# Performance work log

Hardware: AMD Instinct MI355X
Metric: run time of the kernel (lower is better)

The kernel has to match this reference:

```python
import jax, jax.numpy as jnp
import numpy as np

N_NODES = 100000
N_EDGES = 3200000
IN_DIM = 256
HID_DIM = 64
OUT_DIM = 64


def setup_inputs() -> dict:
    key = jax.random.key(0)
    k1, k2, k3, k4, k5, k6 = jax.random.split(key, 6)
    x = jax.random.normal(k1, (N_NODES, IN_DIM), dtype=jnp.float32)
    edge_index = jax.random.randint(k2, (2, N_EDGES), 0, N_NODES, dtype=jnp.int32)
    # Glorot-style init for the two GCNConv layers (PyG default: glorot weight, zero bias)
    W1 = jax.random.normal(k3, (IN_DIM, HID_DIM), dtype=jnp.float32) * (1.0 / np.sqrt(IN_DIM))
    b1 = jnp.zeros((HID_DIM,), dtype=jnp.float32)
    W2 = jax.random.normal(k4, (HID_DIM, OUT_DIM), dtype=jnp.float32) * (1.0 / np.sqrt(HID_DIM))
    b2 = jnp.zeros((OUT_DIM,), dtype=jnp.float32)
    return {"x": x, "edge_index": edge_index, "W1": W1, "b1": b1, "W2": W2, "b2": b2}


def _gcn_conv(x, src, dst, deg_inv_sqrt, W, b, n):
    # PyG GCNConv: h = x W; out_i = sum_j norm_ij * h_j + b, with symmetric norm
    h = x @ W                                   # (n, d_out) small GEMM
    norm = deg_inv_sqrt[src] * deg_inv_sqrt[dst]  # (E+n,)
    msg = norm[:, None] * h[src]                # gather (E+n, d_out)
    agg = jax.ops.segment_sum(msg, dst, num_segments=n)  # scatter-add
    return agg + b


def reference(x, edge_index, W1, b1, W2, b2):
    n = x.shape[0]
    loops = jnp.arange(n, dtype=edge_index.dtype)
    src = jnp.concatenate([edge_index[0], loops])
    dst = jnp.concatenate([edge_index[1], loops])
    # degree on destination (col) with added self-loops, weight 1.0
    deg = jax.ops.segment_sum(jnp.ones_like(dst, dtype=x.dtype), dst, num_segments=n)
    deg_inv_sqrt = jnp.where(deg > 0, jax.lax.rsqrt(deg), 0.0)
    h = jax.nn.relu(_gcn_conv(x, src, dst, deg_inv_sqrt, W1, b1, n))
    return _gcn_conv(h, src, dst, deg_inv_sqrt, W2, b2, n)
```

## Files before the change

kernel.cpp:

```cpp
#include <hip/hip_runtime.h>
#include <cstdint>
#include <cstddef>


#define BIN_SHIFT 7
#define BIN_NODES 128
#define MAX_BINS 1024
#define SUP_SHIFT 11
#define FINE_PER_SUP 16
#define NSUP_MAX 64
#define SCAP 56
#define SRC_BITS 17
#define SRC_MASK ((1 << SRC_BITS) - 1)

typedef unsigned short ushort_t;

typedef __attribute__((ext_vector_type(8))) short bf16x8;
typedef __attribute__((ext_vector_type(4))) float f32x4;

union FragB {
  uint4 u;
  bf16x8 b;
};

__device__ __forceinline__ float4 bfq2f4(uint2 p) {
  float4 r;
  r.x = __uint_as_float(p.x << 16);
  r.y = __uint_as_float(p.x & 0xFFFF0000u);
  r.z = __uint_as_float(p.y << 16);
  r.w = __uint_as_float(p.y & 0xFFFF0000u);
  return r;
}
__device__ __forceinline__ unsigned f2bf(float f) {
  unsigned u = __float_as_uint(f);
  return (u + 0x7FFFu + ((u >> 16) & 1u)) >> 16;
}
__device__ __forceinline__ uint2 f42bfq(float4 f) {
  uint2 r;
  r.x = f2bf(f.x) | (f2bf(f.y) << 16);
  r.y = f2bf(f.z) | (f2bf(f.w) << 16);
  return r;
}

__global__ void zero_int(int* __restrict__ p, int n) {
  int i = blockIdx.x * blockDim.x + threadIdx.x;
  if (i < n) p[i] = 0;
}

__global__ __launch_bounds__(256) void bin_count(const int* __restrict__ dst, int E, int nbins,
                                                 int* __restrict__ binCnt) {
  __shared__ int h[MAX_BINS];
  for (int i = threadIdx.x; i < nbins; i += 256) h[i] = 0;
  __syncthreads();
  int stride = gridDim.x * 256;
  for (int e = blockIdx.x * 256 + threadIdx.x; e < E; e += stride)
    atomicAdd(&h[dst[e] >> BIN_SHIFT], 1);
  __syncthreads();
  for (int i = threadIdx.x; i < nbins; i += 256)
    if (h[i]) atomicAdd(&binCnt[i], h[i]);
}

__global__ __launch_bounds__(256) void bin_scan(const int* __restrict__ binCnt, int nbins, int E,
                                                int* __restrict__ binStart,
                                                int* __restrict__ binCursor,
                                                int* __restrict__ supCursor) {
  __shared__ int s[256];
  int t = threadIdx.x;
  int c[4];
  int sum = 0;
#pragma unroll
  for (int i = 0; i < 4; i++) {
    int idx = t * 4 + i;
    c[i] = (idx < nbins) ? binCnt[idx] : 0;
    sum += c[i];
  }
  int v = sum;
  s[t] = v;
  __syncthreads();
  for (int d = 1; d < 256; d <<= 1) {
    int add = (t >= d) ? s[t - d] : 0;
    __syncthreads();
    s[t] += add;
    __syncthreads();
  }
  int run = s[t] - v;
#pragma unroll
  for (int i = 0; i < 4; i++) {
    int idx = t * 4 + i;
    if (idx < nbins) {
      binStart[idx] = run;
      binCursor[idx] = run;
      if ((idx & (FINE_PER_SUP - 1)) == 0) supCursor[idx >> 4] = run;
      run += c[i];
    }
  }
  if (t == 0) binStart[nbins] = E;
}

__global__ __launch_bounds__(256) void super_fill(const int* __restrict__ src,
                                                  const int* __restrict__ dst, int E, int nsup,
                                                  int* __restrict__ supCursor,
                                                  unsigned* __restrict__ supbuf) {
  __shared__ unsigned stage[NSUP_MAX * SCAP];
  __shared__ int lcnt[NSUP_MAX], lbase[NSUP_MAX], lscan[NSUP_MAX + 1];
  int chunk = (E + gridDim.x - 1) / gridDim.x;
  int c0 = blockIdx.x * chunk;
  int c1 = min(E, c0 + chunk);
  for (int t0 = c0; t0 < c1; t0 += 2048) {
    int t1 = min(c1, t0 + 2048);
    if (threadIdx.x < nsup) lcnt[threadIdx.x] = 0;
    __syncthreads();
    for (int e = t0 + threadIdx.x; e < t1; e += 256) {
      int d = dst[e];
      int sb = d >> SUP_SHIFT;
      unsigned v = ((unsigned)(d & ((1 << SUP_SHIFT) - 1)) << SRC_BITS) | (unsigned)src[e];
      int idx = atomicAdd(&lcnt[sb], 1);
      if (idx < SCAP)
        stage[sb * SCAP + idx] = v;
      else {
        int g = atomicAdd(&supCursor[sb], 1);
        supbuf[g] = v;
      }
    }
    __syncthreads();
    if (threadIdx.x < nsup) {
      int c = min(lcnt[threadIdx.x], SCAP);
      lcnt[threadIdx.x] = c;
      lbase[threadIdx.x] = c ? atomicAdd(&supCursor[threadIdx.x], c) : 0;
    }
    __syncthreads();
    if (threadIdx.x == 0) {
      int r = 0;
      for (int i = 0; i < nsup; i++) {
        lscan[i] = r;
        r += lcnt[i];
      }
      lscan[nsup] = r;
    }
    __syncthreads();
    int total = lscan[nsup];
    for (int j = threadIdx.x; j < total; j += 256) {
      int lo = 0, hi = nsup;
      while (hi - lo > 1) {
        int mid = (lo + hi) >> 1;
        if (lscan[mid] <= j)
          lo = mid;
        else
          hi = mid;
      }
      int off = j - lscan[lo];
      supbuf[lbase[lo] + off] = stage[lo * SCAP + off];
    }
    __syncthreads();
  }
}

__global__ __launch_bounds__(256) void fine_fill(const unsigned* __restrict__ supbuf,
                                                 const int* __restrict__ binStart, int nbins,
                                                 int* __restrict__ binCursor,
                                                 unsigned* __restrict__ binbuf) {
  __shared__ int lcnt[FINE_PER_SUP], lbase[FINE_PER_SUP];
  int sb = blockIdx.x >> 3, p = blockIdx.x & 7;
  int seg0 = binStart[sb << 4];
  int seg1 = binStart[min((sb + 1) << 4, nbins)];
  int part = (seg1 - seg0 + 7) >> 3;
  int c0 = seg0 + p * part;
  int c1 = min(seg1, c0 + part);
  if (threadIdx.x < FINE_PER_SUP) lcnt[threadIdx.x] = 0;
  __syncthreads();
  for (int i = c0 + threadIdx.x; i < c1; i += 256) atomicAdd(&lcnt[supbuf[i] >> 24], 1);
  __syncthreads();
  if (threadIdx.x < FINE_PER_SUP) {
    int c = lcnt[threadIdx.x];
    lbase[threadIdx.x] = c ? atomicAdd(&binCursor[(sb << 4) + threadIdx.x], c) : 0;
    lcnt[threadIdx.x] = 0;
  }
  __syncthreads();
  for (int i = c0 + threadIdx.x; i < c1; i += 256) {
    unsigned v = supbuf[i];
    unsigned dls = v >> SRC_BITS;
    int f = dls >> BIN_SHIFT;
    unsigned vf = ((dls & (BIN_NODES - 1)) << SRC_BITS) | (v & SRC_MASK);
    int idx = lbase[f] + atomicAdd(&lcnt[f], 1);
    binbuf[idx] = vf;
  }
}

__global__ __launch_bounds__(256) void node_count_dis(const unsigned* __restrict__ binbuf,
                                                      const int* __restrict__ binStart, int N,
                                                      int* __restrict__ count,
                                                      float* __restrict__ dis) {
  __shared__ int cnt[BIN_NODES];
  int b = blockIdx.x;
  int nodeBase = b << BIN_SHIFT;
  if (threadIdx.x < BIN_NODES) cnt[threadIdx.x] = 0;
  __syncthreads();
  int s0 = binStart[b], s1 = binStart[b + 1];
  for (int i = s0 + threadIdx.x; i < s1; i += 256) atomicAdd(&cnt[binbuf[i] >> SRC_BITS], 1);
  __syncthreads();
  if (threadIdx.x < BIN_NODES) {
    int node = nodeBase + threadIdx.x;
    if (node < N) {
      int c = cnt[threadIdx.x];
      count[node] = c;
      dis[node] = rsqrtf((float)(c + 1));
    }
  }
}

__global__ __launch_bounds__(256) void bin_csr(const unsigned* __restrict__ binbuf,
                                               const int* __restrict__ binStart,
                                               const int* __restrict__ count, int N, int E,
                                               int* __restrict__ rowptr, int* __restrict__ col) {
  __shared__ int cur[BIN_NODES];
  __shared__ int pref[BIN_NODES];
  int b = blockIdx.x, t = threadIdx.x;
  int nodeBase = b << BIN_SHIFT;
  int c = 0;
  if (t < BIN_NODES) {
    int node = nodeBase + t;
    c = (node < N) ? count[node] : 0;
    pref[t] = c;
  }
  __syncthreads();
  for (int d = 1; d < BIN_NODES; d <<= 1) {
    int add = (t < BIN_NODES && t >= d) ? pref[t - d] : 0;
    __syncthreads();
    if (t < BIN_NODES) pref[t] += add;
    __syncthreads();
  }
  int s0 = binStart[b];
  if (t < BIN_NODES) {
    int node = nodeBase + t;
    if (node < N) {
      int ex = s0 + pref[t] - c;
      rowptr[node] = ex;
      cur[t] = ex;
    }
  }
  if (b == 0 && t == 255) rowptr[N] = E;
  __syncthreads();
  int s1 = binStart[b + 1];
  for (int i = s0 + t; i < s1; i += 256) {
    unsigned v = binbuf[i];
    int slot = atomicAdd(&cur[v >> SRC_BITS], 1);
    col[slot] = v & SRC_MASK;
  }
}

__global__ __launch_bounds__(256) void wsplit(const float* __restrict__ W1,
                                              const float* __restrict__ W2,
                                              ushort_t* __restrict__ wt1,
                                              ushort_t* __restrict__ wt2) {
  int i = blockIdx.x * 256 + threadIdx.x;
  const float* W;
  ushort_t* wt;
  int K, idx;
  if (i < 256 * 64) {
    W = W1; wt = wt1; K = 256; idx = i;
  } else if (i < 256 * 64 + 64 * 64) {
    W = W2; wt = wt2; K = 64; idx = i - 256 * 64;
  } else
    return;
  int n = idx & 63, k = idx >> 6;
  float f = W[k * 64 + n];
  unsigned u = __float_as_uint(f);
  unsigned hb = u & 0xFFFF0000u;
  float lo = f - __uint_as_float(hb);
  wt[(size_t)n * K + k] = (ushort_t)(u >> 16);
  wt[(size_t)64 * K + (size_t)n * K + k] = (ushort_t)(__float_as_uint(lo) >> 16);
}

__device__ __forceinline__ void split8(const float* __restrict__ xp, uint4& xh, uint4& xl) {
  float f[8];
  *(float4*)&f[0] = *(const float4*)xp;
  *(float4*)&f[4] = *(const float4*)(xp + 4);
  unsigned hw[4], lw[4];
#pragma unroll
  for (int p = 0; p < 4; p++) {
    unsigned ua = __float_as_uint(f[2 * p]);
    unsigned ub = __float_as_uint(f[2 * p + 1]);
    unsigned ha = ua & 0xFFFF0000u;
    unsigned hb = ub & 0xFFFF0000u;
    float la = f[2 * p] - __uint_as_float(ha);
    float lb = f[2 * p + 1] - __uint_as_float(hb);
    hw[p] = (ua >> 16) | hb;
    lw[p] = (__float_as_uint(la) >> 16) | (__float_as_uint(lb) & 0xFFFF0000u);
  }
  xh = make_uint4(hw[0], hw[1], hw[2], hw[3]);
  xl = make_uint4(lw[0], lw[1], lw[2], lw[3]);
}

template <int K, bool ABF16>
__global__ __launch_bounds__(256) void gemm_mfma(const void* __restrict__ Av,
                                                 const ushort_t* __restrict__ Wt,
                                                 uint2* __restrict__ Cb, int M) {
  const int lane = threadIdx.x & 63;
  const int wv = threadIdx.x >> 6;
  const int l15 = lane & 15;
  const int lq = lane >> 4;
  const int m0 = blockIdx.x * 128 + wv * 32;

  const ushort_t* __restrict__ Wlo = Wt + (size_t)64 * K;

  f32x4 acc[2][4];
#pragma unroll
  for (int a = 0; a < 2; a++)
#pragma unroll
    for (int b = 0; b < 4; b++) acc[a][b] = (f32x4){0.f, 0.f, 0.f, 0.f};

  int node[2], ncl[2];
#pragma unroll
  for (int mt = 0; mt < 2; mt++) {
    node[mt] = m0 + mt * 16 + l15;
    ncl[mt] = node[mt] < M ? node[mt] : (M - 1);
  }

#pragma unroll 2
  for (int kt = 0; kt < K / 32; kt++) {
    const int kb = kt * 32 + lq * 8;
    FragB wh[4], wl[4];
#pragma unroll
    for (int nt = 0; nt < 4; nt++) {
      wh[nt].u = *(const uint4*)(Wt + (size_t)(nt * 16 + l15) * K + kb);
      wl[nt].u = *(const uint4*)(Wlo + (size_t)(nt * 16 + l15) * K + kb);
    }
#pragma unroll
    for (int mt = 0; mt < 2; mt++) {
      if (ABF16) {
        FragB xa;
        xa.u = *(const uint4*)((const ushort_t*)Av + (size_t)ncl[mt] * K + kb);
#pragma unroll
        for (int nt = 0; nt < 4; nt++) {
          acc[mt][nt] =
              __builtin_amdgcn_mfma_f32_16x16x32_bf16(wh[nt].b, xa.b, acc[mt][nt], 0, 0, 0);
          acc[mt][nt] =
              __builtin_amdgcn_mfma_f32_16x16x32_bf16(wl[nt].b, xa.b, acc[mt][nt], 0, 0, 0);
        }
      } else {
        FragB xh, xl;
        split8((const float*)Av + (size_t)ncl[mt] * K + kb, xh.u, xl.u);
#pragma unroll
        for (int nt = 0; nt < 4; nt++) {
          acc[mt][nt] =
              __builtin_amdgcn_mfma_f32_16x16x32_bf16(wh[nt].b, xh.b, acc[mt][nt], 0, 0, 0);
          acc[mt][nt] =
              __builtin_amdgcn_mfma_f32_16x16x32_bf16(wl[nt].b, xh.b, acc[mt][nt], 0, 0, 0);
          acc[mt][nt] =
              __builtin_amdgcn_mfma_f32_16x16x32_bf16(wh[nt].b, xl.b, acc[mt][nt], 0, 0, 0);
        }
      }
    }
  }

#pragma unroll
  for (int mt = 0; mt < 2; mt++) {
    if (node[mt] < M) {
      uint2* cp = Cb + (size_t)node[mt] * 16 + lq;
#pragma unroll
      for (int nt = 0; nt < 4; nt++) {
        float4 o = make_float4(acc[mt][nt][0], acc[mt][nt][1], acc[mt][nt][2], acc[mt][nt][3]);
        cp[nt * 4] = f42bfq(o);
      }
    }
  }
}

template <bool OUTBF>
__global__ __launch_bounds__(256) void agg_kernel(
    const uint2* __restrict__ h, const int* __restrict__ rowptr, const int* __restrict__ col,
    const float* __restrict__ dis, const float* __restrict__ bias, void* __restrict__ outv,
    int N, int relu) {
  int wid = (blockIdx.x * blockDim.x + threadIdx.x) >> 6;
  if (wid >= N) return;
  int lane = threadIdx.x & 63;
  int sub = lane & 15;
  int quarter = lane >> 4;

  int start = rowptr[wid], end = rowptr[wid + 1];
  float di = dis[wid];

  float4 a0 = make_float4(0.f, 0.f, 0.f, 0.f), a1 = a0, a2 = a0, a3 = a0;
  {
    float4 self = bfq2f4(h[(size_t)wid * 16 + sub]);
    if (quarter == 0) {
      a0.x = di * self.x;
      a0.y = di * self.y;
      a0.z = di * self.z;
      a0.w = di * self.w;
    }
  }

  for (int base = start; base < end; base += 64) {
    int e = base + lane;
    int sj = 0;
    float wj = 0.f;
    if (e < end) {
      sj = col[e];
      wj = dis[sj];
    }
    int cnt = end - base;
    if (cnt > 64) cnt = 64;
    int rounds = (cnt + 3) >> 2;
    int t = 0;
    for (; t + 4 <= rounds; t += 4) {
      int i0 = 4 * t + quarter;
      int s0 = __shfl(sj, i0), s1 = __shfl(sj, i0 + 4), s2 = __shfl(sj, i0 + 8),
          s3 = __shfl(sj, i0 + 12);
      float w0 = __shfl(wj, i0), w1 = __shfl(wj, i0 + 4), w2 = __shfl(wj, i0 + 8),
            w3 = __shfl(wj, i0 + 12);
      float4 g0 = bfq2f4(h[(size_t)s0 * 16 + sub]);
      float4 g1 = bfq2f4(h[(size_t)s1 * 16 + sub]);
      float4 g2 = bfq2f4(h[(size_t)s2 * 16 + sub]);
      float4 g3 = bfq2f4(h[(size_t)s3 * 16 + sub]);
      a0.x += w0 * g0.x; a0.y += w0 * g0.y; a0.z += w0 * g0.z; a0.w += w0 * g0.w;
      a1.x += w1 * g1.x; a1.y += w1 * g1.y; a1.z += w1 * g1.z; a1.w += w1 * g1.w;
      a2.x += w2 * g2.x; a2.y += w2 * g2.y; a2.z += w2 * g2.z; a2.w += w2 * g2.w;
      a3.x += w3 * g3.x; a3.y += w3 * g3.y; a3.z += w3 * g3.z; a3.w += w3 * g3.w;
    }
    for (; t < rounds; t++) {
      int i0 = 4 * t + quarter;
      int s0 = __shfl(sj, i0);
      float w0 = __shfl(wj, i0);
      float4 g0 = bfq2f4(h[(size_t)s0 * 16 + sub]);
      a0.x += w0 * g0.x; a0.y += w0 * g0.y; a0.z += w0 * g0.z; a0.w += w0 * g0.w;
    }
  }

  float sx = (a0.x + a1.x) + (a2.x + a3.x);
  float sy = (a0.y + a1.y) + (a2.y + a3.y);
  float sz = (a0.z + a1.z) + (a2.z + a3.z);
  float sw = (a0.w + a1.w) + (a2.w + a3.w);
  sx += __shfl_down(sx, 32); sy += __shfl_down(sy, 32);
  sz += __shfl_down(sz, 32); sw += __shfl_down(sw, 32);
  sx += __shfl_down(sx, 16); sy += __shfl_down(sy, 16);
  sz += __shfl_down(sz, 16); sw += __shfl_down(sw, 16);
  if (quarter == 0) {
    float4 bv = ((const float4*)bias)[sub];
    float4 o = make_float4(di * sx + bv.x, di * sy + bv.y, di * sz + bv.z, di * sw + bv.w);
    if (relu) {
      o.x = fmaxf(o.x, 0.f);
      o.y = fmaxf(o.y, 0.f);
      o.z = fmaxf(o.z, 0.f);
      o.w = fmaxf(o.w, 0.f);
    }
    if (OUTBF)
      ((uint2*)outv)[(size_t)wid * 16 + sub] = f42bfq(o);
    else
      ((float4*)outv)[(size_t)wid * 16 + sub] = o;
  }
}

extern "C" void kernel_launch(void* const* d_in, const int* in_sizes, int n_in,
                              void* d_out, int out_size, void* d_ws, size_t ws_size,
                              hipStream_t stream) {
  const float* x = (const float*)d_in[0];
  const int* ei = (const int*)d_in[1];
  const float* W1 = (const float*)d_in[2];
  const float* b1 = (const float*)d_in[3];
  const float* W2 = (const float*)d_in[4];
  const float* b2 = (const float*)d_in[5];

  const int IN = 256;
  const int E = in_sizes[1] / 2;
  const int N = in_sizes[0] / IN;
  const int* src = ei;
  const int* dst = ei + E;
  const int nbins = (N + BIN_NODES - 1) >> BIN_SHIFT;
  const int nsup = (N + (1 << SUP_SHIFT) - 1) >> SUP_SHIFT;

  char* ws = (char*)d_ws;
  size_t off = 0;
  auto alloc = [&](size_t bytes) -> void* {
    void* p = ws + off;
    off += (bytes + 255) & ~(size_t)255;
    return p;
  };
  int* count = (int*)alloc((size_t)N * 4);
  int* rowptr = (int*)alloc((size_t)(N + 1) * 4);
  float* dis = (float*)alloc((size_t)N * 4);
  int* binCnt = (int*)alloc(MAX_BINS * 4);
  int* binStart = (int*)alloc((MAX_BINS + 1) * 4);
  int* binCursor = (int*)alloc(MAX_BINS * 4);
  int* supCursor = (int*)alloc(NSUP_MAX * 4);
  int* col = (int*)alloc((size_t)E * 4);
  unsigned* supbuf = (unsigned*)col;
  uint2* out1 = (uint2*)alloc((size_t)N * 64 * 2);
  size_t big = ((size_t)E * 4 > (size_t)N * 128) ? (size_t)E * 4 : (size_t)N * 128;
  unsigned* binbuf = (unsigned*)alloc(big);
  uint2* h = (uint2*)binbuf;
  ushort_t* wt1 = (ushort_t*)alloc((size_t)2 * 64 * 256 * 2);
  ushort_t* wt2 = (ushort_t*)alloc((size_t)2 * 64 * 64 * 2);
  float* outf = (float*)d_out;

  zero_int<<<(nbins + 255) / 256, 256, 0, stream>>>(binCnt, nbins);
  bin_count<<<1024, 256, 0, stream>>>(dst, E, nbins, binCnt);
  bin_scan<<<1, 256, 0, stream>>>(binCnt, nbins, E, binStart, binCursor, supCursor);
  super_fill<<<512, 256, 0, stream>>>(src, dst, E, nsup, supCursor, supbuf);
  fine_fill<<<nsup * 8, 256, 0, stream>>>(supbuf, binStart, nbins, binCursor, binbuf);
  node_count_dis<<<nbins, 256, 0, stream>>>(binbuf, binStart, N, count, dis);
  bin_csr<<<nbins, 256, 0, stream>>>(binbuf, binStart, count, N, E, rowptr, col);
  wsplit<<<(256 * 64 + 64 * 64 + 255) / 256, 256, 0, stream>>>(W1, W2, wt1, wt2);

  gemm_mfma<256, false><<<(N + 127) / 128, 256, 0, stream>>>(x, wt1, h, N);
  agg_kernel<true><<<(N + 3) / 4, 256, 0, stream>>>(h, rowptr, col, dis, b1, out1, N, 1);
  gemm_mfma<64, true><<<(N + 127) / 128, 256, 0, stream>>>(out1, wt2, h, N);
  agg_kernel<false><<<(N + 3) / 4, 256, 0, stream>>>(h, rowptr, col, dis, b2, outf, N, 0);
}
```

Before: 476.6 us.

## Software-pipeline operand loads in MFMA GEMM and set occupancy bound

The fp32-input GEMM path now double-buffers the high weight fragments and prefetches the activation rows two K-steps ahead in registers, so global loads overlap the split and MFMA work. It also reorders the MFMAs to reuse each weight fragment across both M tiles. The bf16-input path hoists all K-step loads ahead of the MFMA chain. Launch bounds now request 3 blocks per CU, which caps registers against the larger register footprint and risks spills.

Result: no change. 473.9 us (-0.6%).

```diff
diff --git a/kernel.cpp b/kernel.cpp
--- a/kernel.cpp
+++ b/kernel.cpp
@@ -271,30 +271,26 @@
   wt[(size_t)64 * K + (size_t)n * K + k] = (ushort_t)(__float_as_uint(lo) >> 16);
 }
 
-__device__ __forceinline__ void split8(const float* __restrict__ xp, uint4& xh, uint4& xl) {
-  float f[8];
-  *(float4*)&f[0] = *(const float4*)xp;
-  *(float4*)&f[4] = *(const float4*)(xp + 4);
+__device__ __forceinline__ void split8u(uint4 a, uint4 b, uint4& xh, uint4& xl) {
+  unsigned ua[8] = {a.x, a.y, a.z, a.w, b.x, b.y, b.z, b.w};
   unsigned hw[4], lw[4];
 #pragma unroll
   for (int p = 0; p < 4; p++) {
-    unsigned ua = __float_as_uint(f[2 * p]);
-    unsigned ub = __float_as_uint(f[2 * p + 1]);
-    unsigned ha = ua & 0xFFFF0000u;
-    unsigned hb = ub & 0xFFFF0000u;
-    float la = f[2 * p] - __uint_as_float(ha);
-    float lb = f[2 * p + 1] - __uint_as_float(hb);
-    hw[p] = (ua >> 16) | hb;
-    lw[p] = (__float_as_uint(la) >> 16) | (__float_as_uint(lb) & 0xFFFF0000u);
+    unsigned u0 = ua[2 * p], u1 = ua[2 * p + 1];
+    unsigned h0 = u0 & 0xFFFF0000u, h1 = u1 & 0xFFFF0000u;
+    float l0 = __uint_as_float(u0) - __uint_as_float(h0);
+    float l1 = __uint_as_float(u1) - __uint_as_float(h1);
+    hw[p] = (u0 >> 16) | h1;
+    lw[p] = (__float_as_uint(l0) >> 16) | (__float_as_uint(l1) & 0xFFFF0000u);
   }
   xh = make_uint4(hw[0], hw[1], hw[2], hw[3]);
   xl = make_uint4(lw[0], lw[1], lw[2], lw[3]);
 }
 
 template <int K, bool ABF16>
-__global__ __launch_bounds__(256) void gemm_mfma(const void* __restrict__ Av,
-                                                 const ushort_t* __restrict__ Wt,
-                                                 uint2* __restrict__ Cb, int M) {
+__global__ __launch_bounds__(256, 3) void gemm_mfma(const void* __restrict__ Av,
+                                                    const ushort_t* __restrict__ Wt,
+                                                    uint2* __restrict__ Cb, int M) {
   const int lane = threadIdx.x & 63;
   const int wv = threadIdx.x >> 6;
   const int l15 = lane & 15;
@@ -316,39 +312,88 @@
     ncl[mt] = node[mt] < M ? node[mt] : (M - 1);
   }
 
-#pragma unroll 2
-  for (int kt = 0; kt < K / 32; kt++) {
-    const int kb = kt * 32 + lq * 8;
-    FragB wh[4], wl[4];
-#pragma unroll
-    for (int nt = 0; nt < 4; nt++) {
-      wh[nt].u = *(const uint4*)(Wt + (size_t)(nt * 16 + l15) * K + kb);
-      wl[nt].u = *(const uint4*)(Wlo + (size_t)(nt * 16 + l15) * K + kb);
-    }
-#pragma unroll
-    for (int mt = 0; mt < 2; mt++) {
-      if (ABF16) {
-        FragB xa;
-        xa.u = *(const uint4*)((const ushort_t*)Av + (size_t)ncl[mt] * K + kb);
+  if (ABF16) {
+    constexpr int NT = K / 32;
+    FragB xa[NT][2], wh[NT][4], wl[NT][4];
+#pragma unroll
+    for (int t = 0; t < NT; t++)
+#pragma unroll
+      for (int mt = 0; mt < 2; mt++)
+        xa[t][mt].u = *(const uint4*)((const ushort_t*)Av + (size_t)ncl[mt] * K + t * 32 + lq * 8);
+#pragma unroll
+    for (int t = 0; t < NT; t++)
+#pragma unroll
+      for (int nt = 0; nt < 4; nt++) {
+        wh[t][nt].u = *(const uint4*)(Wt + (size_t)(nt * 16 + l15) * K + t * 32 + lq * 8);
+        wl[t][nt].u = *(const uint4*)(Wlo + (size_t)(nt * 16 + l15) * K + t * 32 + lq * 8);
+      }
+#pragma unroll
+    for (int t = 0; t < NT; t++)
+#pragma unroll
+      for (int mt = 0; mt < 2; mt++)
 #pragma unroll
         for (int nt = 0; nt < 4; nt++) {
           acc[mt][nt] =
-              __builtin_amdgcn_mfma_f32_16x16x32_bf16(wh[nt].b, xa.b, acc[mt][nt], 0, 0, 0);
+              __builtin_amdgcn_mfma_f32_16x16x32_bf16(wh[t][nt].b, xa[t][mt].b, acc[mt][nt], 0, 0, 0);
           acc[mt][nt] =
-              __builtin_amdgcn_mfma_f32_16x16x32_bf16(wl[nt].b, xa.b, acc[mt][nt], 0, 0, 0);
+              __builtin_amdgcn_mfma_f32_16x16x32_bf16(wl[t][nt].b, xa[t][mt].b, acc[mt][nt], 0, 0, 0);
         }
-      } else {
-        FragB xh, xl;
-        split8((const float*)Av + (size_t)ncl[mt] * K + kb, xh.u, xl.u);
-#pragma unroll
-        for (int nt = 0; nt < 4; nt++) {
-          acc[mt][nt] =
-              __builtin_amdgcn_mfma_f32_16x16x32_bf16(wh[nt].b, xh.b, acc[mt][nt], 0, 0, 0);
-          acc[mt][nt] =
-              __builtin_amdgcn_mfma_f32_16x16x32_bf16(wl[nt].b, xh.b, acc[mt][nt], 0, 0, 0);
-          acc[mt][nt] =
-              __builtin_amdgcn_mfma_f32_16x16x32_bf16(wh[nt].b, xl.b, acc[mt][nt], 0, 0, 0);
+  } else {
+    constexpr int NT = K / 32;
+    const float* __restrict__ A = (const float*)Av;
+    uint4 xp[2][2][2];
+    FragB wh[2][4];
+    FragB wlc[4];
+
+#pragma unroll
+    for (int nt = 0; nt < 4; nt++)
+      wh[0][nt].u = *(const uint4*)(Wt + (size_t)(nt * 16 + l15) * K + lq * 8);
+#pragma unroll
+    for (int t = 0; t < 2; t++)
+#pragma unroll
+      for (int mt = 0; mt < 2; mt++) {
+        const float* p = A + (size_t)ncl[mt] * K + t * 32 + lq * 8;
+        xp[t][mt][0] = *(const uint4*)p;
+        xp[t][mt][1] = *(const uint4*)(p + 4);
+      }
+
+#pragma unroll
+    for (int kt = 0; kt < NT; kt++) {
+      const int cs = kt & 1;
+      const int kb = kt * 32 + lq * 8;
+      if (kt + 1 < NT) {
+        const int kbn = (kt + 1) * 32 + lq * 8;
+#pragma unroll
+        for (int nt = 0; nt < 4; nt++)
+          wh[cs ^ 1][nt].u = *(const uint4*)(Wt + (size_t)(nt * 16 + l15) * K + kbn);
+      }
+#pragma unroll
+      for (int nt = 0; nt < 4; nt++)
+        wlc[nt].u = *(const uint4*)(Wlo + (size_t)(nt * 16 + l15) * K + kb);
+      uint4 c0a = xp[cs][0][0], c0b = xp[cs][0][1];
+      uint4 c1a = xp[cs][1][0], c1b = xp[cs][1][1];
+      if (kt + 2 < NT) {
+#pragma unroll
+        for (int mt = 0; mt < 2; mt++) {
+          const float* p = A + (size_t)ncl[mt] * K + (kt + 2) * 32 + lq * 8;
+          xp[cs][mt][0] = *(const uint4*)p;
+          xp[cs][mt][1] = *(const uint4*)(p + 4);
         }
+      }
+      FragB xh0, xl0, xh1, xl1;
+      split8u(c0a, c0b, xh0.u, xl0.u);
+      split8u(c1a, c1b, xh1.u, xl1.u);
+#pragma unroll
+      for (int nt = 0; nt < 4; nt++) {
+        acc[0][nt] = __builtin_amdgcn_mfma_f32_16x16x32_bf16(wh[cs][nt].b, xh0.b, acc[0][nt], 0, 0, 0);
+        acc[0][nt] = __builtin_amdgcn_mfma_f32_16x16x32_bf16(wh[cs][nt].b, xl0.b, acc[0][nt], 0, 0, 0);
+        acc[1][nt] = __builtin_amdgcn_mfma_f32_16x16x32_bf16(wh[cs][nt].b, xh1.b, acc[1][nt], 0, 0, 0);
+        acc[1][nt] = __builtin_amdgcn_mfma_f32_16x16x32_bf16(wh[cs][nt].b, xl1.b, acc[1][nt], 0, 0, 0);
+      }
+#pragma unroll
+      for (int nt = 0; nt < 4; nt++) {
+        acc[0][nt] = __builtin_amdgcn_mfma_f32_16x16x32_bf16(wlc[nt].b, xh0.b, acc[0][nt], 0, 0, 0);
+        acc[1][nt] = __builtin_amdgcn_mfma_f32_16x16x32_bf16(wlc[nt].b, xh1.b, acc[1][nt], 0, 0, 0);
       }
     }
   }
```
